# Optimization experiments

Measured on AMD Instinct MI355X. Metric: run time of the kernel, lower is better.

## Reference

```python
import jax, jax.numpy as jnp
import numpy as np

B, L, H, HEADS, N_NODE = 1024, 200, 128, 8, 200000
MAXN = L + 1  # max_n_node
D = H // HEADS
EPS = 1e-12


def setup_inputs() -> dict:
    key = jax.random.key(0)
    ks = jax.random.split(key, 20)
    lengths = jax.random.randint(ks[0], (B,), 1, L + 1)
    mask = (jnp.arange(L)[None, :] < lengths[:, None]).astype(jnp.int32)  # contiguous 1s
    alias_inputs = jax.random.randint(ks[1], (B, L), 0, MAXN)
    items = jax.random.randint(ks[2], (B, MAXN), 0, N_NODE)

    def lin_w(k, o, i):
        return (jax.random.normal(k, (o, i), jnp.float32) * 0.1)

    inp = dict(
        alias_inputs=alias_inputs,
        items=items,
        mask=mask,
        emb_W=jax.random.normal(ks[3], (N_NODE, H), jnp.float32) * 0.1,
        # LastAttenion params
        W0=lin_w(ks[4], H, H), b0=jax.random.normal(ks[5], (H,), jnp.float32) * 0.1,
        W1=lin_w(ks[6], H, H), b1=jax.random.normal(ks[7], (H,), jnp.float32) * 0.1,
        W2=lin_w(ks[8], H, H), b2=jax.random.normal(ks[9], (H,), jnp.float32) * 0.1,
        # linear_q[0] (last_k = 1)
        Wq=lin_w(ks[10], H, H), bq=jax.random.normal(ks[11], (H,), jnp.float32) * 0.1,
        # linear_transform (2H -> H)
        Wt=lin_w(ks[12], H, 2 * H), bt=jax.random.normal(ks[13], (H,), jnp.float32) * 0.1,
        ln_g=jax.random.normal(ks[14], (H,), jnp.float32) * 0.1,
        ln_b=jax.random.normal(ks[15], (H,), jnp.float32) * 0.1,
    )
    return inp


def reference(alias_inputs, items, mask, emb_W, W0, b0, W1, b1, W2, b2, Wq, bq, Wt, bt, ln_g, ln_b):
    maskf = mask.astype(jnp.float32)
    # hidden = normalize(embedding(items)); dropout off (eval)
    hidden = emb_W[items]                                                  # [B, MAXN, H]
    hidden = hidden / (jnp.linalg.norm(hidden, axis=-1, keepdims=True) + EPS)
    # per-batch gather: seq_hidden[b, t] = hidden[b, alias_inputs[b, t]]
    seq = jnp.take_along_axis(hidden, alias_inputs[..., None], axis=1)     # [B, L, H]
    seq = seq * maskf[..., None]
    seq = seq / (jnp.linalg.norm(seq, axis=-1, keepdims=True) + EPS)
    # compute_scores
    lengths = mask.sum(1)
    last_idx = lengths - 1                                                 # >= 0 (lengths >= 1)
    ht_last = seq[jnp.arange(B), last_idx]                                 # [B, H]  (ht0 too)
    hts = (ht_last @ Wq.T + bq)[:, None, :]                                # [B, 1, H]
    # torch.norm over dim=1 (size 1) == elementwise abs
    hts = hts / (jnp.linalg.norm(hts, axis=1, keepdims=True) + EPS)
    # LastAttenion (last_k = 1, no lp-pool, eval dropout off)
    q0 = (hts @ W0.T + b0).reshape(B * HEADS, 1, D)                        # [B*h, 1, d]
    q1 = (seq @ W1.T + b1).reshape(B * HEADS, L, D)                        # [B*h, L, d]
    q2 = (seq @ W2.T + b2).reshape(B, L, HEADS, D)                         # [B, L, h, d]
    alpha = jax.nn.sigmoid(jnp.einsum('bkd,bld->bkl', q0, q1))             # [B*h, 1, L]
    alpha = alpha.reshape(B, HEADS, L).transpose(0, 2, 1)                  # [B, L, h]
    alpha = jax.nn.softmax(2.0 * alpha, axis=1)
    a = jnp.sum((alpha[..., None] * q2).reshape(B, L, H) * maskf[..., None], axis=1)  # [B, H]
    # layernorm eps=1e-8
    mu = a.mean(-1, keepdims=True)
    var = ((a - mu) ** 2).mean(-1, keepdims=True)
    a = (a - mu) / jnp.sqrt(var + 1e-8) * ln_g + ln_b
    a = jnp.concatenate([a, ht_last], axis=1) @ Wt.T + bt                  # [B, H]
    # norm=True branch
    a = a / (jnp.linalg.norm(a, axis=1, keepdims=True) + EPS)
    b = emb_W[1:]
    b = b / (jnp.linalg.norm(b, axis=1, keepdims=True) + EPS)
    return a, b.T                                                          # [B,H], [H, N_NODE-1]
```

## Files before the change

kernel.cpp:

```cpp
#include <hip/hip_runtime.h>
#include <math.h>

typedef unsigned int uint;
typedef unsigned short ushort;

__device__ __forceinline__ float b2f(ushort u){
  union { uint i; float f; } v; v.i = ((uint)u) << 16; return v.f;
}
__device__ __forceinline__ ushort f2b(float f){
  union { float f; uint i; } v; v.f = f;
  uint i = v.i;
  i += 0x7fffu + ((i >> 16) & 1u);
  return (ushort)(i >> 16);
}
__device__ __forceinline__ float wred(float v){
  #pragma unroll
  for (int s = 32; s > 0; s >>= 1) v += __shfl_xor(v, s, 64);
  return v;
}
__device__ __forceinline__ float gred16(float v){
  v += __shfl_xor(v, 1, 64);
  v += __shfl_xor(v, 2, 64);
  v += __shfl_xor(v, 4, 64);
  v += __shfl_xor(v, 8, 64);
  return v;
}
__device__ __forceinline__ float sane(float v){ return isfinite(v) ? v : 0.f; }
__device__ __forceinline__ int iclamp(int v, int lo, int hi){ return v < lo ? lo : (v > hi ? hi : v); }
__device__ __forceinline__ void cp8(float d[8], const float s[8]){
  #pragma unroll
  for (int e = 0; e < 8; ++e) d[e] = s[e];
}

__device__ __forceinline__ void load_raw8(const void* emb, int isf, int it, int p, float x[8]){
  if (it >= 0){
    if (isf){
      const float4* q = (const float4*)((const float*)emb + (size_t)it * 128);
      float4 u = q[p * 2], u2 = q[p * 2 + 1];
      x[0] = u.x; x[1] = u.y; x[2] = u.z; x[3] = u.w;
      x[4] = u2.x; x[5] = u2.y; x[6] = u2.z; x[7] = u2.w;
    } else {
      uint4 u = ((const uint4*)((const ushort*)emb + (size_t)it * 128))[p];
      x[0] = b2f((ushort)u.x); x[1] = b2f((ushort)(u.x >> 16));
      x[2] = b2f((ushort)u.y); x[3] = b2f((ushort)(u.y >> 16));
      x[4] = b2f((ushort)u.z); x[5] = b2f((ushort)(u.z >> 16));
      x[6] = b2f((ushort)u.w); x[7] = b2f((ushort)(u.w >> 16));
    }
  } else {
    #pragma unroll
    for (int e = 0; e < 8; ++e) x[e] = 0.f;
  }
}

__device__ __forceinline__ int detect_isf(const void* emb, int t, int* s_flag){
  if (t == 0) *s_flag = 0;
  __syncthreads();
  if (t < 64){
    uint4 u = ((const uint4*)emb)[t];
    uint w[4] = { u.x, u.y, u.z, u.w };
    int bad = 0;
    #pragma unroll
    for (int e = 0; e < 4; ++e){
      float v0 = fabsf(b2f((ushort)w[e]));
      float v1 = fabsf(b2f((ushort)(w[e] >> 16)));
      if (!(v0 <= 1e4f) || !(v1 <= 1e4f)) bad = 1;
    }
    if (bad) *s_flag = 1;
  }
  __syncthreads();
  return *s_flag;
}

#define OUTB 131072

#define C_W0T 0
#define C_W1  16384
#define C_W2T 32768
#define C_WQT 49152
#define C_WTT 65536
#define C_B0  98304
#define C_B1  98432
#define C_B2  98560
#define C_BQ  98688
#define C_BT  98816
#define C_G   98944
#define C_BB  99072
#define C_TOT 99200

#define KMAIN_SMEM 22784

__global__ __launch_bounds__(256) void k_bout(
    const void* __restrict__ emb,
    const void* W0, const void* b0, const void* W1, const void* b1,
    const void* W2, const void* b2, const void* Wq, const void* bq,
    const void* Wt, const void* bt, const void* g, const void* bb,
    float* __restrict__ wts, void* __restrict__ outv){
  __shared__ float tile[64 * 129];
  __shared__ int s_flag;
  const int t = threadIdx.x, gid = t >> 4, p = t & 15;
  const int base = blockIdx.x * 64;
  const int isf = detect_isf(emb, t, &s_flag);
  for (int i = gid; i < 64; i += 16){
    int gi = base + i;
    if (gi < 199999){
      float x[8];
      if (isf){
        const float4* q = (const float4*)((const float*)emb + (size_t)(gi + 1) * 128);
        float4 u = q[p * 2], u2 = q[p * 2 + 1];
        x[0] = u.x; x[1] = u.y; x[2] = u.z; x[3] = u.w;
        x[4] = u2.x; x[5] = u2.y; x[6] = u2.z; x[7] = u2.w;
      } else {
        uint4 u = ((const uint4*)((const ushort*)emb + (size_t)(gi + 1) * 128))[p];
        x[0] = b2f((ushort)u.x); x[1] = b2f((ushort)(u.x >> 16));
        x[2] = b2f((ushort)u.y); x[3] = b2f((ushort)(u.y >> 16));
        x[4] = b2f((ushort)u.z); x[5] = b2f((ushort)(u.z >> 16));
        x[6] = b2f((ushort)u.w); x[7] = b2f((ushort)(u.w >> 16));
      }
      float ss = 0.f;
      #pragma unroll
      for (int e = 0; e < 8; ++e) ss += x[e] * x[e];
      ss = gred16(ss);
      float inv = 1.f / (sqrtf(ss) + 1e-12f);
      #pragma unroll
      for (int e = 0; e < 8; ++e) tile[i * 129 + p * 8 + e] = x[e] * inv;
    }
  }
  __syncthreads();
  for (int it = 0; it < 32; ++it){
    int idx = it * 256 + t;
    int h = idx >> 6, n = idx & 63;
    int gi = base + n;
    if (gi < 199999){
      float val = sane(tile[n * 129 + h]);
      if (isf) ((float*)outv)[OUTB + (size_t)h * 199999 + gi] = val;
      else     ((ushort*)outv)[OUTB + (size_t)h * 199999 + gi] = f2b(val);
    }
  }
  int j = blockIdx.x * 256 + t;
  if (blockIdx.x < 388 && j < C_TOT){
    const void* src; int si;
    if (j < 16384)      { int k = j >> 7, h = j & 127; src = W0; si = h * 128 + k; }
    else if (j < 32768) { src = W1; si = j - 16384; }
    else if (j < 49152) { int i = j - 32768; int k = i >> 7, h = i & 127; src = W2; si = h * 128 + k; }
    else if (j < 65536) { int i = j - 49152; int k = i >> 7, h = i & 127; src = Wq; si = h * 128 + k; }
    else if (j < 98304) { int i = j - 65536; int k = i >> 7, h = i & 127; src = Wt; si = h * 256 + k; }
    else {
      int i = j - 98304; int arr = i >> 7;
      const void* tab[7] = { b0, b1, b2, bq, bt, g, bb };
      src = tab[arr]; si = i & 127;
    }
    wts[j] = isf ? ((const float*)src)[si] : b2f(((const ushort*)src)[si]);
  }
}

__global__ __launch_bounds__(256) void k_main(
    const int* __restrict__ alias_, const int* __restrict__ items,
    const int* __restrict__ mask, const void* __restrict__ emb,
    const float* __restrict__ wts, void* __restrict__ outv){
  extern __shared__ __align__(16) char dsm[];
  __shared__ int s_flag;
  __shared__ float s_X0[128], s_ht[128], s_a[128], s_hts[128];
  __shared__ float s_c1[64];
  __shared__ float s_T[8], s_Tp[64];
  __shared__ float s_red[16];
  __shared__ float s_nrm[200];
  __shared__ int   s_it[200];
  __shared__ int   s_item;

  const int t = threadIdx.x;
  const int isf = detect_isf(emb, t, &s_flag);
  const int b = blockIdx.x;

  ushort* s_w1p   = (ushort*)dsm;
  float*  s_part  = (float*)dsm;
  float*  s_alpha = (float*)(dsm + 16384);

  const int wv = t >> 6, gid = t >> 4, p = t & 15, lane = t & 63;
  const int mbase = b * 200;

  int mv = 0;
  if (t < 200){
    mv = mask[mbase + t];
    int a = mv ? iclamp(alias_[mbase + t], 0, 200) : 0;
    s_it[t] = mv ? iclamp(items[b * 201 + a], 0, 199999) : -1;
  }
  float lv = wred((float)mv);
  if ((t & 63) == 0) s_red[t >> 6] = lv;
  __syncthreads();

  float xc[8], xn1[8];
  load_raw8(emb, isf, s_it[gid], p, xc);
  load_raw8(emb, isf, s_it[gid + 16], p, xn1);

  const int len = iclamp((int)(s_red[0] + s_red[1] + s_red[2] + s_red[3] + 0.5f), 1, 200);
  if (t == 0){
    int a = iclamp(alias_[mbase + len - 1], 0, 200);
    s_item = iclamp(items[b * 201 + a], 0, 199999);
  }
  __syncthreads();

  float v = 0.f;
  if (t < 128)
    v = isf ? ((const float*)emb)[(size_t)s_item * 128 + t]
            : b2f(((const ushort*)emb)[(size_t)s_item * 128 + t]);
  float ss = wred(v * v);
  if ((t & 63) == 0) s_red[4 + (t >> 6)] = ss;
  __syncthreads();
  v = v / (sqrtf(s_red[4] + s_red[5]) + 1e-12f);
  float ss2 = wred(v * v);
  if ((t & 63) == 0) s_red[8 + (t >> 6)] = ss2;
  __syncthreads();
  v = v / (sqrtf(s_red[8] + s_red[9]) + 1e-12f);
  if (t < 128) s_ht[t] = v;
  __syncthreads();

  if (t < 128){
    double d0 = 0.0, d1 = 0.0, d2 = 0.0, d3 = 0.0;
    for (int k = 0; k < 128; k += 4){
      d0 += (double)wts[C_WQT + (k    ) * 128 + t] * (double)s_ht[k    ];
      d1 += (double)wts[C_WQT + (k + 1) * 128 + t] * (double)s_ht[k + 1];
      d2 += (double)wts[C_WQT + (k + 2) * 128 + t] * (double)s_ht[k + 2];
      d3 += (double)wts[C_WQT + (k + 3) * 128 + t] * (double)s_ht[k + 3];
    }
    float a = (float)((double)wts[C_BQ + t] + ((d0 + d1) + (d2 + d3)));
    s_hts[t] = a / (fabsf(a) + 1e-12f);
  }
  __syncthreads();
  if (t < 128){
    float a0 = 0.f, a1 = 0.f, a2 = 0.f, a3 = 0.f;
    for (int k = 0; k < 128; k += 4){
      a0 += wts[C_W0T + (k    ) * 128 + t] * s_hts[k    ];
      a1 += wts[C_W0T + (k + 1) * 128 + t] * s_hts[k + 1];
      a2 += wts[C_W0T + (k + 2) * 128 + t] * s_hts[k + 2];
      a3 += wts[C_W0T + (k + 3) * 128 + t] * s_hts[k + 3];
    }
    s_X0[t] = wts[C_B0 + t] + ((a0 + a1) + (a2 + a3));
  }
  __syncthreads();
  if (t < 64){
    int head = t >> 3, j = t & 7;
    float c = 0.f;
    #pragma unroll
    for (int d = 0; d < 16; ++d) c += s_X0[head * 16 + d] * wts[C_B1 + j * 16 + d];
    s_c1[t] = c;
  }

  __syncthreads();
  for (int idx = t; idx < 8192; idx += 256){
    int hj = idx >> 7, k = idx & 127, head = hj >> 3, j = hj & 7;
    float acc = 0.f;
    const float* w1r = wts + C_W1 + (j * 16) * 128 + k;
    #pragma unroll
    for (int d = 0; d < 16; ++d) acc += s_X0[head * 16 + d] * w1r[d * 128];
    s_w1p[hj * 128 + k] = f2b(acc);
  }
  __syncthreads();

  {
    float xt[8];
    for (int r = gid; r < 200; r += 16){
      int rn = r + 32;
      load_raw8(emb, isf, rn < 200 ? s_it[rn] : -1, p, xt);

      int head = r / 25, lb = (r % 25) * 8;
      uint4 wu[8];
      #pragma unroll
      for (int j = 0; j < 8; ++j)
        wu[j] = *(const uint4*)(s_w1p + (head * 8 + j) * 128 + p * 8);

      float ssr = 0.f;
      #pragma unroll
      for (int e = 0; e < 8; ++e) ssr += xc[e] * xc[e];
      ssr = gred16(ssr);
      float inv = 1.f / (sqrtf(ssr) + 1e-12f);
      #pragma unroll
      for (int e = 0; e < 8; ++e) xc[e] *= inv;
      if (p == 0) s_nrm[r] = inv;

      #pragma unroll
      for (int j = 0; j < 8; ++j){
        float dot = xc[0] * b2f((ushort)wu[j].x) + xc[1] * b2f((ushort)(wu[j].x >> 16))
                  + xc[2] * b2f((ushort)wu[j].y) + xc[3] * b2f((ushort)(wu[j].y >> 16))
                  + xc[4] * b2f((ushort)wu[j].z) + xc[5] * b2f((ushort)(wu[j].z >> 16))
                  + xc[6] * b2f((ushort)wu[j].w) + xc[7] * b2f((ushort)(wu[j].w >> 16));
        dot = gred16(dot);
        if (p == 0){
          float logit = s_c1[head * 8 + j] + dot;
          s_alpha[(lb + j) * 8 + head] = 2.f / (1.f + expf(-logit));
        }
      }
      cp8(xc, xn1); cp8(xn1, xt);
    }
  }
  __syncthreads();

  {
    int head = t >> 5, l32 = t & 31;
    float vals[7]; float mx = -1e30f;
    #pragma unroll
    for (int i = 0; i < 7; ++i){
      int l = l32 + 32 * i;
      float xx = (l < 200) ? s_alpha[l * 8 + head] : -1e30f;
      vals[i] = xx; mx = fmaxf(mx, xx);
    }
    #pragma unroll
    for (int s = 16; s > 0; s >>= 1) mx = fmaxf(mx, __shfl_xor(mx, s, 64));
    float sum = 0.f; float e[7];
    #pragma unroll
    for (int i = 0; i < 7; ++i){
      int l = l32 + 32 * i;
      float ex = (l < 200) ? expf(vals[i] - mx) : 0.f;
      e[i] = ex; sum += ex;
    }
    #pragma unroll
    for (int s = 16; s > 0; s >>= 1) sum += __shfl_xor(sum, s, 64);
    float inv = 1.f / sum;
    #pragma unroll
    for (int i = 0; i < 7; ++i){
      int l = l32 + 32 * i;
      if (l < 200) s_alpha[l * 8 + head] = e[i] * inv;
    }
  }
  __syncthreads();

  if (t < 64){
    int h = t & 7, seg = t >> 3;
    int l0 = seg * 25, l1 = l0 + 25; if (l1 > len) l1 = len;
    float s = 0.f;
    for (int l = l0; l < l1; ++l) s += s_alpha[l * 8 + h];
    s_Tp[t] = s;
  }
  __syncthreads();
  if (t < 8){
    float s = 0.f;
    #pragma unroll
    for (int seg = 0; seg < 8; ++seg) s += s_Tp[seg * 8 + t];
    s_T[t] = s;
  }

  float acc[64];
  #pragma unroll
  for (int e = 0; e < 64; ++e) acc[e] = 0.f;
  {
    float ha[8], hb[8], ht8[8];
    load_raw8(emb, isf, s_it[gid], p, ha);
    load_raw8(emb, isf, gid + 16 < 200 ? s_it[gid + 16] : -1, p, hb);
    for (int l = gid; l < 200; l += 16){
      int lc = l + 32;
      load_raw8(emb, isf, lc < 200 ? s_it[lc] : -1, p, ht8);
      if (s_it[l] >= 0){
        float nm = s_nrm[l];
        float x[8];
        #pragma unroll
        for (int e = 0; e < 8; ++e) x[e] = ha[e] * nm;
        float4 a0 = *(const float4*)(s_alpha + l * 8);
        float4 a1 = *(const float4*)(s_alpha + l * 8 + 4);
        float al[8] = { a0.x, a0.y, a0.z, a0.w, a1.x, a1.y, a1.z, a1.w };
        #pragma unroll
        for (int h = 0; h < 8; ++h)
          #pragma unroll
          for (int e = 0; e < 8; ++e) acc[h * 8 + e] += al[h] * x[e];
      }
      cp8(ha, hb); cp8(hb, ht8);
    }
  }
  #pragma unroll
  for (int e = 0; e < 64; ++e){
    float vv = acc[e];
    vv += __shfl_xor(vv, 16, 64);
    vv += __shfl_xor(vv, 32, 64);
    acc[e] = vv;
  }
  __syncthreads();
  if (lane < 16){
    #pragma unroll
    for (int h = 0; h < 8; ++h)
      #pragma unroll
      for (int e = 0; e < 8; ++e)
        s_part[wv * 1024 + h * 128 + p * 8 + e] = acc[h * 8 + e];
  }
  __syncthreads();
  for (int i = t; i < 1024; i += 256)
    s_part[i] = s_part[i] + s_part[1024 + i] + s_part[2048 + i] + s_part[3072 + i];
  __syncthreads();

  float araw = 0.f;
  if (t < 128){
    int head = t >> 4;
    const float* hl = &s_part[head * 128];
    float a0 = 0.f, a1 = 0.f, a2 = 0.f, a3 = 0.f;
    for (int k = 0; k < 128; k += 4){
      a0 += hl[k    ] * wts[C_W2T + (k    ) * 128 + t];
      a1 += hl[k + 1] * wts[C_W2T + (k + 1) * 128 + t];
      a2 += hl[k + 2] * wts[C_W2T + (k + 2) * 128 + t];
      a3 += hl[k + 3] * wts[C_W2T + (k + 3) * 128 + t];
    }
    araw = wts[C_B2 + t] * s_T[head] + ((a0 + a1) + (a2 + a3));
  }
  float v1 = wred(t < 128 ? araw : 0.f);
  if ((t & 63) == 0) s_red[t >> 6] = v1;
  __syncthreads();
  float mu = (s_red[0] + s_red[1]) * 0.0078125f;
  float dd = (t < 128) ? (araw - mu) : 0.f;
  float v2 = wred(dd * dd);
  if ((t & 63) == 0) s_red[4 + (t >> 6)] = v2;
  __syncthreads();
  float var = (s_red[4] + s_red[5]) * 0.0078125f;
  if (t < 128)
    s_a[t] = dd / sqrtf(var + 1e-8f) * wts[C_G + t] + wts[C_BB + t];
  __syncthreads();

  float o = 0.f;
  if (t < 128){
    float o0 = 0.f, o1 = 0.f, o2 = 0.f, o3 = 0.f;
    for (int k = 0; k < 128; k += 2){
      o0 += s_a[k    ] * wts[C_WTT + (k      ) * 128 + t];
      o1 += s_a[k + 1] * wts[C_WTT + (k + 1  ) * 128 + t];
      o2 += s_ht[k   ] * wts[C_WTT + (128 + k) * 128 + t];
      o3 += s_ht[k+ 1] * wts[C_WTT + (129 + k) * 128 + t];
    }
    o = wts[C_BT + t] + ((o0 + o1) + (o2 + o3));
  }
  float v3 = wred(t < 128 ? o * o : 0.f);
  if ((t & 63) == 0) s_red[8 + (t >> 6)] = v3;
  __syncthreads();
  float nrm = sqrtf(s_red[8] + s_red[9]);
  if (t < 128){
    float val = sane(o / (nrm + 1e-12f));
    if (isf) ((float*)outv)[b * 128 + t] = val;
    else     ((ushort*)outv)[b * 128 + t] = f2b(val);
  }
}

extern "C" void kernel_launch(void* const* d_in, const int* in_sizes, int n_in,
                              void* d_out, int out_size, void* d_ws, size_t ws_size,
                              hipStream_t stream){
  const int* alias_ = (const int*)d_in[0];
  const int* items  = (const int*)d_in[1];
  const int* mask   = (const int*)d_in[2];
  const void* emb = d_in[3];
  const void* W0  = d_in[4];
  const void* b0  = d_in[5];
  const void* W1  = d_in[6];
  const void* b1  = d_in[7];
  const void* W2  = d_in[8];
  const void* b2_ = d_in[9];
  const void* Wq  = d_in[10];
  const void* bq  = d_in[11];
  const void* Wt  = d_in[12];
  const void* bt  = d_in[13];
  const void* g_  = d_in[14];
  const void* bb_ = d_in[15];

  char* ws = (char*)d_ws;
  float* wts = (float*)ws;

  static int g_attr_done = 0;
  if (!g_attr_done){
    hipFuncSetAttribute(reinterpret_cast<const void*>(k_main),
                        hipFuncAttributeMaxDynamicSharedMemorySize, KMAIN_SMEM);
    g_attr_done = 1;
  }

  k_bout<<<dim3(3125), dim3(256), 0,          stream>>>(emb, W0, b0, W1, b1,
                                              W2, b2_, Wq, bq, Wt, bt, g_, bb_,
                                              wts, d_out);
  k_main<<<dim3(1024), dim3(256), KMAIN_SMEM, stream>>>(alias_, items, mask, emb,
                                              wts, d_out);
}
```

Before: 378.6 us.

## Pair transposed output stores, widen bout blocks, and rebalance k_main matvecs

k_bout now handles 128 embedding rows per block in two 64-row passes, halving the grid. It writes the transposed normalized output as paired 2-element nontemporal stores when alignment allows, to cut store instructions and cache pollution on the large write. In k_main, the W1 head projection is restructured so each thread reuses one weight load across four heads. The first gathered rows are prefetched before the softmax stage, and the final Wt matvec is split across all 256 threads. Several matvec loops also get unroll pragmas, which may raise register pressure.

```diff
diff --git a/kernel.cpp b/kernel.cpp
--- a/kernel.cpp
+++ b/kernel.cpp
@@ -3,6 +3,7 @@
 
 typedef unsigned int uint;
 typedef unsigned short ushort;
+typedef float vf2 __attribute__((ext_vector_type(2)));
 
 __device__ __forceinline__ float b2f(ushort u){
   union { uint i; float f; } v; v.i = ((uint)u) << 16; return v.f;
@@ -89,6 +90,8 @@
 
 #define KMAIN_SMEM 22784
 
+#define NB_BOUT 1563
+
 __global__ __launch_bounds__(256) void k_bout(
     const void* __restrict__ emb,
     const void* W0, const void* b0, const void* W1, const void* b1,
@@ -98,42 +101,55 @@
   __shared__ float tile[64 * 129];
   __shared__ int s_flag;
   const int t = threadIdx.x, gid = t >> 4, p = t & 15;
-  const int base = blockIdx.x * 64;
   const int isf = detect_isf(emb, t, &s_flag);
-  for (int i = gid; i < 64; i += 16){
-    int gi = base + i;
-    if (gi < 199999){
-      float x[8];
+  const int base = blockIdx.x * 128;
+
+  for (int pass = 0; pass < 2; ++pass){
+    const int pb = base + pass * 64;
+    if (pass) __syncthreads();
+    for (int i = gid; i < 64; i += 16){
+      int gi = pb + i;
+      if (gi < 199999){
+        float x[8];
+        load_raw8(emb, isf, gi + 1, p, x);
+        float ss = 0.f;
+        #pragma unroll
+        for (int e = 0; e < 8; ++e) ss += x[e] * x[e];
+        ss = gred16(ss);
+        float inv = 1.f / (sqrtf(ss) + 1e-12f);
+        #pragma unroll
+        for (int e = 0; e < 8; ++e) tile[i * 129 + p * 8 + e] = x[e] * inv;
+      }
+    }
+    __syncthreads();
+    #pragma unroll
+    for (int it = 0; it < 16; ++it){
+      int idx = it * 256 + t;
+      int h = idx >> 5, n2 = (idx & 31) * 2;
+      int gi = pb + n2;
       if (isf){
-        const float4* q = (const float4*)((const float*)emb + (size_t)(gi + 1) * 128);
-        float4 u = q[p * 2], u2 = q[p * 2 + 1];
-        x[0] = u.x; x[1] = u.y; x[2] = u.z; x[3] = u.w;
-        x[4] = u2.x; x[5] = u2.y; x[6] = u2.z; x[7] = u2.w;
+        float* op = (float*)outv + OUTB + (size_t)h * 199999 + gi;
+        float w0 = sane(tile[n2 * 129 + h]);
+        float w1 = sane(tile[(n2 + 1) * 129 + h]);
+        if (!(h & 1) && gi + 1 < 199999){
+          vf2 w2; w2.x = w0; w2.y = w1;
+          __builtin_nontemporal_store(w2, (vf2*)op);
+        } else {
+          if (gi < 199999)     __builtin_nontemporal_store(w0, op);
+          if (gi + 1 < 199999) __builtin_nontemporal_store(w1, op + 1);
+        }
       } else {
-        uint4 u = ((const uint4*)((const ushort*)emb + (size_t)(gi + 1) * 128))[p];
-        x[0] = b2f((ushort)u.x); x[1] = b2f((ushort)(u.x >> 16));
-        x[2] = b2f((ushort)u.y); x[3] = b2f((ushort)(u.y >> 16));
-        x[4] = b2f((ushort)u.z); x[5] = b2f((ushort)(u.z >> 16));
-        x[6] = b2f((ushort)u.w); x[7] = b2f((ushort)(u.w >> 16));
+        ushort* op = (ushort*)outv + OUTB + (size_t)h * 199999 + gi;
+        ushort w0 = f2b(sane(tile[n2 * 129 + h]));
+        ushort w1 = f2b(sane(tile[(n2 + 1) * 129 + h]));
+        if (!(h & 1) && gi + 1 < 199999){
+          uint w = (uint)w0 | ((uint)w1 << 16);
+          __builtin_nontemporal_store(w, (uint*)op);
+        } else {
+          if (gi < 199999)     __builtin_nontemporal_store(w0, op);
+          if (gi + 1 < 199999) __builtin_nontemporal_store(w1, op + 1);
+        }
       }
-      float ss = 0.f;
-      #pragma unroll
-      for (int e = 0; e < 8; ++e) ss += x[e] * x[e];
-      ss = gred16(ss);
-      float inv = 1.f / (sqrtf(ss) + 1e-12f);
-      #pragma unroll
-      for (int e = 0; e < 8; ++e) tile[i * 129 + p * 8 + e] = x[e] * inv;
-    }
-  }
-  __syncthreads();
-  for (int it = 0; it < 32; ++it){
-    int idx = it * 256 + t;
-    int h = idx >> 6, n = idx & 63;
-    int gi = base + n;
-    if (gi < 199999){
-      float val = sane(tile[n * 129 + h]);
-      if (isf) ((float*)outv)[OUTB + (size_t)h * 199999 + gi] = val;
-      else     ((ushort*)outv)[OUTB + (size_t)h * 199999 + gi] = f2b(val);
     }
   }
   int j = blockIdx.x * 256 + t;
@@ -163,6 +179,7 @@
   __shared__ float s_c1[64];
   __shared__ float s_T[8], s_Tp[64];
   __shared__ float s_red[16];
+  __shared__ float s_fp[256];
   __shared__ float s_nrm[200];
   __shared__ int   s_it[200];
   __shared__ int   s_item;
@@ -216,6 +233,7 @@
 
   if (t < 128){
     double d0 = 0.0, d1 = 0.0, d2 = 0.0, d3 = 0.0;
+    #pragma unroll 2
     for (int k = 0; k < 128; k += 4){
       d0 += (double)wts[C_WQT + (k    ) * 128 + t] * (double)s_ht[k    ];
       d1 += (double)wts[C_WQT + (k + 1) * 128 + t] * (double)s_ht[k + 1];
@@ -228,6 +246,7 @@
   __syncthreads();
   if (t < 128){
     float a0 = 0.f, a1 = 0.f, a2 = 0.f, a3 = 0.f;
+    #pragma unroll 4
     for (int k = 0; k < 128; k += 4){
       a0 += wts[C_W0T + (k    ) * 128 + t] * s_hts[k    ];
       a1 += wts[C_W0T + (k + 1) * 128 + t] * s_hts[k + 1];
@@ -246,13 +265,25 @@
   }
 
   __syncthreads();
-  for (int idx = t; idx < 8192; idx += 256){
-    int hj = idx >> 7, k = idx & 127, head = hj >> 3, j = hj & 7;
-    float acc = 0.f;
-    const float* w1r = wts + C_W1 + (j * 16) * 128 + k;
-    #pragma unroll
-    for (int d = 0; d < 16; ++d) acc += s_X0[head * 16 + d] * w1r[d * 128];
-    s_w1p[hj * 128 + k] = f2b(acc);
+  {
+    const int k = t & 127, half = t >> 7;
+    const int h0 = half * 4;
+    #pragma unroll
+    for (int j = 0; j < 8; ++j){
+      float s0 = 0.f, s1 = 0.f, s2 = 0.f, s3 = 0.f;
+      #pragma unroll
+      for (int d = 0; d < 16; ++d){
+        float w = wts[C_W1 + (j * 16 + d) * 128 + k];
+        s0 += s_X0[(h0    ) * 16 + d] * w;
+        s1 += s_X0[(h0 + 1) * 16 + d] * w;
+        s2 += s_X0[(h0 + 2) * 16 + d] * w;
+        s3 += s_X0[(h0 + 3) * 16 + d] * w;
+      }
+      s_w1p[((h0    ) * 8 + j) * 128 + k] = f2b(s0);
+      s_w1p[((h0 + 1) * 8 + j) * 128 + k] = f2b(s1);
+      s_w1p[((h0 + 2) * 8 + j) * 128 + k] = f2b(s2);
+      s_w1p[((h0 + 3) * 8 + j) * 128 + k] = f2b(s3);
+    }
   }
   __syncthreads();
 
@@ -294,6 +325,10 @@
   }
   __syncthreads();
 
+  float ha[8], hb[8];
+  load_raw8(emb, isf, s_it[gid], p, ha);
+  load_raw8(emb, isf, s_it[gid + 16], p, hb);
+
   {
     int head = t >> 5, l32 = t & 31;
     float vals[7]; float mx = -1e30f;
@@ -342,9 +377,7 @@
   #pragma unroll
   for (int e = 0; e < 64; ++e) acc[e] = 0.f;
   {
-    float ha[8], hb[8], ht8[8];
-    load_raw8(emb, isf, s_it[gid], p, ha);
-    load_raw8(emb, isf, gid + 16 < 200 ? s_it[gid + 16] : -1, p, hb);
+    float ht8[8];
     for (int l = gid; l < 200; l += 16){
       int lc = l + 32;
       load_raw8(emb, isf, lc < 200 ? s_it[lc] : -1, p, ht8);
@@ -389,6 +422,7 @@
     int head = t >> 4;
     const float* hl = &s_part[head * 128];
     float a0 = 0.f, a1 = 0.f, a2 = 0.f, a3 = 0.f;
+    #pragma unroll 8
     for (int k = 0; k < 128; k += 4){
       a0 += hl[k    ] * wts[C_W2T + (k    ) * 128 + t];
       a1 += hl[k + 1] * wts[C_W2T + (k + 1) * 128 + t];
@@ -410,17 +444,23 @@
     s_a[t] = dd / sqrtf(var + 1e-8f) * wts[C_G + t] + wts[C_BB + t];
   __syncthreads();
 
+  {
+    const int h = t & 127;
+    const float* src = (t < 128) ? s_a : s_ht;
+    const int koff = (t < 128) ? 0 : 128;
+    float q0 = 0.f, q1 = 0.f, q2 = 0.f, q3 = 0.f;
+    #pragma unroll 8
+    for (int k = 0; k < 128; k += 4){
+      q0 += src[k    ] * wts[C_WTT + (koff + k    ) * 128 + h];
+      q1 += src[k + 1] * wts[C_WTT + (koff + k + 1) * 128 + h];
+      q2 += src[k + 2] * wts[C_WTT + (koff + k + 2) * 128 + h];
+      q3 += src[k + 3] * wts[C_WTT + (koff + k + 3) * 128 + h];
+    }
+    s_fp[t] = ((q0 + q1) + (q2 + q3));
+  }
+  __syncthreads();
   float o = 0.f;
-  if (t < 128){
-    float o0 = 0.f, o1 = 0.f, o2 = 0.f, o3 = 0.f;
-    for (int k = 0; k < 128; k += 2){
-      o0 += s_a[k    ] * wts[C_WTT + (k      ) * 128 + t];
-      o1 += s_a[k + 1] * wts[C_WTT + (k + 1  ) * 128 + t];
-      o2 += s_ht[k   ] * wts[C_WTT + (128 + k) * 128 + t];
-      o3 += s_ht[k+ 1] * wts[C_WTT + (129 + k) * 128 + t];
-    }
-    o = wts[C_BT + t] + ((o0 + o1) + (o2 + o3));
-  }
+  if (t < 128) o = wts[C_BT + t] + (s_fp[t] + s_fp[128 + t]);
   float v3 = wred(t < 128 ? o * o : 0.f);
   if ((t & 63) == 0) s_red[8 + (t >> 6)] = v3;
   __syncthreads();
@@ -457,14 +497,15 @@
 
   static int g_attr_done = 0;
   if (!g_attr_done){
-    hipFuncSetAttribute(reinterpret_cast<const void*>(k_main),
+    hipError_t e = hipFuncSetAttribute(reinterpret_cast<const void*>(k_main),
                         hipFuncAttributeMaxDynamicSharedMemorySize, KMAIN_SMEM);
+    (void)e;
     g_attr_done = 1;
   }
 
-  k_bout<<<dim3(3125), dim3(256), 0,          stream>>>(emb, W0, b0, W1, b1,
-                                              W2, b2_, Wq, bq, Wt, bt, g_, bb_,
-                                              wts, d_out);
-  k_main<<<dim3(1024), dim3(256), KMAIN_SMEM, stream>>>(alias_, items, mask, emb,
-                                              wts, d_out);
-}
+  k_bout<<<dim3(NB_BOUT), dim3(256), 0,          stream>>>(emb, W0, b0, W1, b1,
+                                                 W2, b2_, Wq, bq, Wt, bt, g_, bb_,
+                                                 wts, d_out);
+  k_main<<<dim3(1024),    dim3(256), KMAIN_SMEM, stream>>>(alias_, items, mask, emb,
+                                                 wts, d_out);
+}
```

New measurement: 417.7 us. 10.3% more time.
